# Performance work log

Hardware: AMD Instinct MI355X
Metric: run time of the kernel (lower is better)

The kernel has to match this reference:

```python
import jax, jax.numpy as jnp
import numpy as np
import math

GRID = 14  # coords run 1..13 -> 13x13 spatial grid
Z = math.exp(math.log(2.0 * math.pi) + 1.0)
EPS = 1e-06

def setup_inputs() -> dict:
    key = jax.random.key(0)
    B, C = 256, 1024
    x = jax.random.normal(key, (B, GRID - 1, GRID - 1, C), dtype=jnp.float32)
    return {"feature_input": x}

def reference(feature_input) -> jnp.ndarray:
    B, H, W, C = feature_input.shape
    f = jax.nn.softmax(feature_input, axis=3)  # softmax over channel dim (dim=3)
    coords = jnp.arange(1, GRID, dtype=jnp.float32)  # [13]
    xv = coords[:, None]  # varies along spatial axis 0 (torch meshgrid 'ij')
    yv = coords[None, :]  # varies along spatial axis 1
    s = f.sum(axis=(1, 2)) + EPS  # [B, C] per-slice mass
    # soft-argmax centroids, [B, C]
    mx = (xv[None, :, :, None] * f).sum(axis=(1, 2)) / s
    my = (yv[None, :, :, None] * f).sum(axis=(1, 2)) / s
    # weighted variances, normalized by 169 and the per-slice mass
    dx2 = (xv[None, :, :, None] - mx[:, None, None, :]) ** 2
    dy2 = (yv[None, :, :, None] - my[:, None, None, :]) ** 2
    x_var = (dx2 * f).sum(axis=(1, 2)) / 169.0 / s
    y_var = (dy2 * f).sum(axis=(1, 2)) / 169.0 / s
    det_xy = (x_var + y_var) ** 2 * Z  # [B, C]
    return det_xy.sum() / B / C
```

## Files before the change

### kernel.cpp

```cpp
#include <hip/hip_runtime.h>

#ifndef __has_builtin
#define __has_builtin(x) 0
#endif

__device__ __forceinline__ float fast_exp2(float x) {
#if __has_builtin(__builtin_amdgcn_exp2f)
    return __builtin_amdgcn_exp2f(x);
#else
    return exp2f(x);
#endif
}

constexpr int   kB      = 256;
constexpr int   kC      = 1024;
constexpr int   kP      = 169;
constexpr int   kRows   = kB * kP;
constexpr float kEps    = 1e-6f;
constexpr float kZ      = 17.079468445347132f;
constexpr float kLog2e  = 1.4426950408889634f;
constexpr float kInv169 = 1.0f / 169.0f;
constexpr float kScale  = 1.0f / (256.0f * 1024.0f);

__global__ __launch_bounds__(256, 4)
void rowsum_kernel(const float* __restrict__ x, float* __restrict__ L)
{
    const int tid  = threadIdx.x;
    const int lane = tid & 63;
    const int wid  = tid >> 6;
    const int row  = blockIdx.x * 4 + wid;

    const float4* __restrict__ src = (const float4*)(x + (size_t)row * kC);
    float4 v0 = src[lane];
    float4 v1 = src[lane + 64];
    float4 v2 = src[lane + 128];
    float4 v3 = src[lane + 192];

    float s =
        (fast_exp2(v0.x * kLog2e) + fast_exp2(v0.y * kLog2e)) +
        (fast_exp2(v0.z * kLog2e) + fast_exp2(v0.w * kLog2e)) +
        (fast_exp2(v1.x * kLog2e) + fast_exp2(v1.y * kLog2e)) +
        (fast_exp2(v1.z * kLog2e) + fast_exp2(v1.w * kLog2e)) +
        (fast_exp2(v2.x * kLog2e) + fast_exp2(v2.y * kLog2e)) +
        (fast_exp2(v2.z * kLog2e) + fast_exp2(v2.w * kLog2e)) +
        (fast_exp2(v3.x * kLog2e) + fast_exp2(v3.y * kLog2e)) +
        (fast_exp2(v3.z * kLog2e) + fast_exp2(v3.w * kLog2e));

    #pragma unroll
    for (int m = 1; m < 64; m <<= 1)
        s += __shfl_xor(s, m);

    if (lane == 0) L[row] = log2f(s);
}

__global__ __launch_bounds__(256, 4)
void moments_kernel(const float* __restrict__ x, const float* __restrict__ L,
                    float* __restrict__ out)
{
    __shared__ float4 sTab[kP];
    __shared__ float  snL[kP];
    __shared__ float  sred[4];

    const int tid  = threadIdx.x;
    const int lane = tid & 63;
    const int wid  = tid >> 6;
    const int b    = blockIdx.x >> 1;
    const int half = blockIdx.x & 1;

    const float* __restrict__ Lb = L + b * kP;
    for (int i = tid; i < kP; i += 256) {
        snL[i] = -Lb[i];
        const int h = i / 13;
        const int w = i - h * 13;
        const float fx = (float)(h + 1);
        const float fy = (float)(w + 1);
        sTab[i] = make_float4(fx, fy, fx * fx, fy * fy);
    }
    __syncthreads();

    const int c0 = half * 512 + 2 * tid;
    const float* __restrict__ xb = x + (size_t)b * kP * kC + c0;

    float A0[2] = {0.f, 0.f}, A1[2] = {0.f, 0.f}, A2[2] = {0.f, 0.f};
    float A3[2] = {0.f, 0.f}, A4[2] = {0.f, 0.f};

    for (int p0 = 0; p0 < 168; p0 += 8) {
        float2 v[8];
        #pragma unroll
        for (int j = 0; j < 8; ++j)
            v[j] = *(const float2*)(xb + (size_t)(p0 + j) * kC);

        #pragma unroll
        for (int j = 0; j < 8; ++j) {
            const int   p  = p0 + j;
            const float nl = snL[p];
            const float4 t = sTab[p];
            const float e0 = fast_exp2(fmaf(v[j].x, kLog2e, nl));
            const float e1 = fast_exp2(fmaf(v[j].y, kLog2e, nl));
            A0[0] += e0;
            A1[0] = fmaf(t.x, e0, A1[0]);
            A2[0] = fmaf(t.y, e0, A2[0]);
            A3[0] = fmaf(t.z, e0, A3[0]);
            A4[0] = fmaf(t.w, e0, A4[0]);
            A0[1] += e1;
            A1[1] = fmaf(t.x, e1, A1[1]);
            A2[1] = fmaf(t.y, e1, A2[1]);
            A3[1] = fmaf(t.z, e1, A3[1]);
            A4[1] = fmaf(t.w, e1, A4[1]);
        }
    }
    {
        const int p = 168;
        const float2 v  = *(const float2*)(xb + (size_t)p * kC);
        const float  nl = snL[p];
        const float4 t  = sTab[p];
        const float e0 = fast_exp2(fmaf(v.x, kLog2e, nl));
        const float e1 = fast_exp2(fmaf(v.y, kLog2e, nl));
        A0[0] += e0; A1[0] = fmaf(t.x, e0, A1[0]); A2[0] = fmaf(t.y, e0, A2[0]);
        A3[0] = fmaf(t.z, e0, A3[0]); A4[0] = fmaf(t.w, e0, A4[0]);
        A0[1] += e1; A1[1] = fmaf(t.x, e1, A1[1]); A2[1] = fmaf(t.y, e1, A2[1]);
        A3[1] = fmaf(t.z, e1, A3[1]); A4[1] = fmaf(t.w, e1, A4[1]);
    }

    float det = 0.f;
    #pragma unroll
    for (int ch = 0; ch < 2; ++ch) {
        const float s   = A0[ch] + kEps;
        const float is  = 1.0f / s;
        const float mx  = A1[ch] * is;
        const float my  = A2[ch] * is;
        const float nx  = A3[ch] - mx * (2.0f * A1[ch] - mx * A0[ch]);
        const float ny  = A4[ch] - my * (2.0f * A2[ch] - my * A0[ch]);
        const float t   = (nx + ny) * is * kInv169;
        det = fmaf(t * t, kZ, det);
    }

    #pragma unroll
    for (int m = 1; m < 64; m <<= 1)
        det += __shfl_xor(det, m);

    if (lane == 0) sred[wid] = det;
    __syncthreads();
    if (tid == 0)
        atomicAdd(out, (sred[0] + sred[1] + sred[2] + sred[3]) * kScale);
}

extern "C" void kernel_launch(void* const* d_in, const int* in_sizes, int n_in,
                              void* d_out, int out_size, void* d_ws, size_t ws_size,
                              hipStream_t stream)
{
    const float* x   = (const float*)d_in[0];
    float*       out = (float*)d_out;
    float*       L   = (float*)d_ws;

    hipMemsetAsync(out, 0, sizeof(float) * (size_t)out_size, stream);
    rowsum_kernel <<<dim3(kRows / 4), dim3(256), 0, stream>>>(x, L);
    moments_kernel<<<dim3(kB * 2),    dim3(256), 0, stream>>>(x, L, out);
}
```

Baseline: 267.0 us.

## Fuse row logsumexp and spatial moments into one per-batch kernel

Replaces the two-kernel pipeline with a single 1024-thread block per batch image. The block first computes the row log-sum-exp values into shared memory, then re-reads the same 676 KB slice (likely hitting cache) to accumulate separable x/y moments. The workspace round-trip and one launch go away, and the position weights are factored per row. The trade-off is only 256 blocks, which may underfill the GPU's CUs, and a serial phase split by a barrier within each block.

New measurement: 263.7 us. No clear change (-1.2%).

```diff
diff --git a/kernel.cpp b/kernel.cpp
--- a/kernel.cpp
+++ b/kernel.cpp
@@ -12,128 +12,98 @@
 #endif
 }
 
+__device__ __forceinline__ float fast_log2(float x) {
+#if __has_builtin(__builtin_amdgcn_logf)
+    return __builtin_amdgcn_logf(x);
+#else
+    return log2f(x);
+#endif
+}
+
 constexpr int   kB      = 256;
 constexpr int   kC      = 1024;
-constexpr int   kP      = 169;
-constexpr int   kRows   = kB * kP;
+constexpr int   kG      = 13;
+constexpr int   kP      = kG * kG;
 constexpr float kEps    = 1e-6f;
 constexpr float kZ      = 17.079468445347132f;
 constexpr float kLog2e  = 1.4426950408889634f;
 constexpr float kInv169 = 1.0f / 169.0f;
 constexpr float kScale  = 1.0f / (256.0f * 1024.0f);
 
-__global__ __launch_bounds__(256, 4)
-void rowsum_kernel(const float* __restrict__ x, float* __restrict__ L)
+__global__ __launch_bounds__(1024, 4)
+void constrain_loss_fused(const float* __restrict__ x, float* __restrict__ out)
 {
-    const int tid  = threadIdx.x;
-    const int lane = tid & 63;
-    const int wid  = tid >> 6;
-    const int row  = blockIdx.x * 4 + wid;
-
-    const float4* __restrict__ src = (const float4*)(x + (size_t)row * kC);
-    float4 v0 = src[lane];
-    float4 v1 = src[lane + 64];
-    float4 v2 = src[lane + 128];
-    float4 v3 = src[lane + 192];
-
-    float s =
-        (fast_exp2(v0.x * kLog2e) + fast_exp2(v0.y * kLog2e)) +
-        (fast_exp2(v0.z * kLog2e) + fast_exp2(v0.w * kLog2e)) +
-        (fast_exp2(v1.x * kLog2e) + fast_exp2(v1.y * kLog2e)) +
-        (fast_exp2(v1.z * kLog2e) + fast_exp2(v1.w * kLog2e)) +
-        (fast_exp2(v2.x * kLog2e) + fast_exp2(v2.y * kLog2e)) +
-        (fast_exp2(v2.z * kLog2e) + fast_exp2(v2.w * kLog2e)) +
-        (fast_exp2(v3.x * kLog2e) + fast_exp2(v3.y * kLog2e)) +
-        (fast_exp2(v3.z * kLog2e) + fast_exp2(v3.w * kLog2e));
-
-    #pragma unroll
-    for (int m = 1; m < 64; m <<= 1)
-        s += __shfl_xor(s, m);
-
-    if (lane == 0) L[row] = log2f(s);
-}
-
-__global__ __launch_bounds__(256, 4)
-void moments_kernel(const float* __restrict__ x, const float* __restrict__ L,
-                    float* __restrict__ out)
-{
-    __shared__ float4 sTab[kP];
-    __shared__ float  snL[kP];
-    __shared__ float  sred[4];
+    __shared__ float snL[kP];
+    __shared__ float sred[16];
 
     const int tid  = threadIdx.x;
     const int lane = tid & 63;
     const int wid  = tid >> 6;
-    const int b    = blockIdx.x >> 1;
-    const int half = blockIdx.x & 1;
+    const int b    = blockIdx.x;
 
-    const float* __restrict__ Lb = L + b * kP;
-    for (int i = tid; i < kP; i += 256) {
-        snL[i] = -Lb[i];
-        const int h = i / 13;
-        const int w = i - h * 13;
-        const float fx = (float)(h + 1);
-        const float fy = (float)(w + 1);
-        sTab[i] = make_float4(fx, fy, fx * fx, fy * fy);
+    const float* __restrict__ xb = x + (size_t)b * kP * kC;
+
+    for (int p = wid; p < kP; p += 16) {
+        const float4* __restrict__ src = (const float4*)(xb + (size_t)p * kC);
+        float4 v0 = src[lane];
+        float4 v1 = src[lane + 64];
+        float4 v2 = src[lane + 128];
+        float4 v3 = src[lane + 192];
+
+        float s =
+            (fast_exp2(v0.x * kLog2e) + fast_exp2(v0.y * kLog2e)) +
+            (fast_exp2(v0.z * kLog2e) + fast_exp2(v0.w * kLog2e)) +
+            (fast_exp2(v1.x * kLog2e) + fast_exp2(v1.y * kLog2e)) +
+            (fast_exp2(v1.z * kLog2e) + fast_exp2(v1.w * kLog2e)) +
+            (fast_exp2(v2.x * kLog2e) + fast_exp2(v2.y * kLog2e)) +
+            (fast_exp2(v2.z * kLog2e) + fast_exp2(v2.w * kLog2e)) +
+            (fast_exp2(v3.x * kLog2e) + fast_exp2(v3.y * kLog2e)) +
+            (fast_exp2(v3.z * kLog2e) + fast_exp2(v3.w * kLog2e));
+
+        #pragma unroll
+        for (int m = 1; m < 64; m <<= 1)
+            s += __shfl_xor(s, m);
+
+        if (lane == 0) snL[p] = -fast_log2(s);
     }
     __syncthreads();
 
-    const int c0 = half * 512 + 2 * tid;
-    const float* __restrict__ xb = x + (size_t)b * kP * kC + c0;
+    const float* __restrict__ xc = xb + tid;
 
-    float A0[2] = {0.f, 0.f}, A1[2] = {0.f, 0.f}, A2[2] = {0.f, 0.f};
-    float A3[2] = {0.f, 0.f}, A4[2] = {0.f, 0.f};
+    float S0 = 0.f, S1x = 0.f, S2x = 0.f, S1y = 0.f, S2y = 0.f;
 
-    for (int p0 = 0; p0 < 168; p0 += 8) {
-        float2 v[8];
+    #pragma unroll
+    for (int h = 0; h < kG; ++h) {
+        const float* __restrict__ row = xc + (size_t)h * kG * kC;
+        float v[kG];
         #pragma unroll
-        for (int j = 0; j < 8; ++j)
-            v[j] = *(const float2*)(xb + (size_t)(p0 + j) * kC);
+        for (int w = 0; w < kG; ++w)
+            v[w] = row[(size_t)w * kC];
 
+        float t0 = 0.f, t1 = 0.f, t2 = 0.f;
         #pragma unroll
-        for (int j = 0; j < 8; ++j) {
-            const int   p  = p0 + j;
-            const float nl = snL[p];
-            const float4 t = sTab[p];
-            const float e0 = fast_exp2(fmaf(v[j].x, kLog2e, nl));
-            const float e1 = fast_exp2(fmaf(v[j].y, kLog2e, nl));
-            A0[0] += e0;
-            A1[0] = fmaf(t.x, e0, A1[0]);
-            A2[0] = fmaf(t.y, e0, A2[0]);
-            A3[0] = fmaf(t.z, e0, A3[0]);
-            A4[0] = fmaf(t.w, e0, A4[0]);
-            A0[1] += e1;
-            A1[1] = fmaf(t.x, e1, A1[1]);
-            A2[1] = fmaf(t.y, e1, A2[1]);
-            A3[1] = fmaf(t.z, e1, A3[1]);
-            A4[1] = fmaf(t.w, e1, A4[1]);
+        for (int w = 0; w < kG; ++w) {
+            const float e = fast_exp2(fmaf(v[w], kLog2e, snL[h * kG + w]));
+            t0 += e;
+            t1 = fmaf((float)(w + 1), e, t1);
+            t2 = fmaf((float)((w + 1) * (w + 1)), e, t2);
         }
-    }
-    {
-        const int p = 168;
-        const float2 v  = *(const float2*)(xb + (size_t)p * kC);
-        const float  nl = snL[p];
-        const float4 t  = sTab[p];
-        const float e0 = fast_exp2(fmaf(v.x, kLog2e, nl));
-        const float e1 = fast_exp2(fmaf(v.y, kLog2e, nl));
-        A0[0] += e0; A1[0] = fmaf(t.x, e0, A1[0]); A2[0] = fmaf(t.y, e0, A2[0]);
-        A3[0] = fmaf(t.z, e0, A3[0]); A4[0] = fmaf(t.w, e0, A4[0]);
-        A0[1] += e1; A1[1] = fmaf(t.x, e1, A1[1]); A2[1] = fmaf(t.y, e1, A2[1]);
-        A3[1] = fmaf(t.z, e1, A3[1]); A4[1] = fmaf(t.w, e1, A4[1]);
+        const float fx = (float)(h + 1);
+        S0  += t0;
+        S1x  = fmaf(fx,      t0, S1x);
+        S2x  = fmaf(fx * fx, t0, S2x);
+        S1y += t1;
+        S2y += t2;
     }
 
-    float det = 0.f;
-    #pragma unroll
-    for (int ch = 0; ch < 2; ++ch) {
-        const float s   = A0[ch] + kEps;
-        const float is  = 1.0f / s;
-        const float mx  = A1[ch] * is;
-        const float my  = A2[ch] * is;
-        const float nx  = A3[ch] - mx * (2.0f * A1[ch] - mx * A0[ch]);
-        const float ny  = A4[ch] - my * (2.0f * A2[ch] - my * A0[ch]);
-        const float t   = (nx + ny) * is * kInv169;
-        det = fmaf(t * t, kZ, det);
-    }
+    const float s   = S0 + kEps;
+    const float is  = 1.0f / s;
+    const float mx  = S1x * is;
+    const float my  = S1y * is;
+    const float nx  = S2x - mx * (2.0f * S1x - mx * S0);
+    const float ny  = S2y - my * (2.0f * S1y - my * S0);
+    const float t   = (nx + ny) * is * kInv169;
+    float det = t * t * kZ;
 
     #pragma unroll
     for (int m = 1; m < 64; m <<= 1)
@@ -141,8 +111,13 @@
 
     if (lane == 0) sred[wid] = det;
     __syncthreads();
-    if (tid == 0)
-        atomicAdd(out, (sred[0] + sred[1] + sred[2] + sred[3]) * kScale);
+    if (wid == 0) {
+        float v = (lane < 16) ? sred[lane] : 0.0f;
+        #pragma unroll
+        for (int m = 1; m < 16; m <<= 1)
+            v += __shfl_xor(v, m);
+        if (lane == 0) atomicAdd(out, v * kScale);
+    }
 }
 
 extern "C" void kernel_launch(void* const* d_in, const int* in_sizes, int n_in,
@@ -151,9 +126,7 @@
 {
     const float* x   = (const float*)d_in[0];
     float*       out = (float*)d_out;
-    float*       L   = (float*)d_ws;
 
     hipMemsetAsync(out, 0, sizeof(float) * (size_t)out_size, stream);
-    rowsum_kernel <<<dim3(kRows / 4), dim3(256), 0, stream>>>(x, L);
-    moments_kernel<<<dim3(kB * 2),    dim3(256), 0, stream>>>(x, L, out);
+    constrain_loss_fused<<<dim3(kB), dim3(1024), 0, stream>>>(x, out);
 }
```
